# Kernel optimization log

Measured on AMD Instinct MI355X. Metric: run time of the kernel, lower is better.

## Reference

```python
import jax, jax.numpy as jnp
import numpy as np
import math

N = 500_000
C_IN = 16
C_OUT = 64
H, W = 256, 256
PE_DIM = 32
BOUNDS = (-1.0, 1.0)
LN_EPS = 1e-5


def setup_inputs() -> dict:
    key = jax.random.key(0)
    ks = jax.random.split(key, 4)
    d_in = C_IN + 6 * PE_DIM  # 208
    pos = jax.random.uniform(ks[0], (N, 3), jnp.float32, minval=-1.0, maxval=1.0)
    features = jax.random.normal(ks[1], (N, C_IN), jnp.float32)
    W1 = jax.random.normal(ks[2], (d_in, C_OUT), jnp.float32) * (1.0 / math.sqrt(d_in))
    b1 = jnp.zeros((C_OUT,), jnp.float32)
    ln_g = jnp.ones((C_OUT,), jnp.float32)
    ln_b = jnp.zeros((C_OUT,), jnp.float32)
    W2 = jax.random.normal(ks[3], (C_OUT, C_OUT), jnp.float32) * (1.0 / math.sqrt(C_OUT))
    b2 = jnp.zeros((C_OUT,), jnp.float32)
    return {"pos": pos, "features": features, "W1": W1, "b1": b1,
            "ln_g": ln_g, "ln_b": ln_b, "W2": W2, "b2": b2,
            "axis1": 0, "axis2": 1}


def _pos_encode(pos):
    # sinusoidal encoding: per spatial dim, sin/cos at PE_DIM frequencies
    scale = BOUNDS[1] - BOUNDS[0]
    freq_bands = jnp.arange(PE_DIM, dtype=jnp.float32) / PE_DIM  # linspace(0,31,32)/32
    freqs = (pos / scale)[..., None] * (2.0 ** freq_bands) * math.pi  # [N,3,PE]
    # ordering per dim: sin_d, cos_d -> [N, 3*2*PE]
    enc = jnp.stack([jnp.sin(freqs), jnp.cos(freqs)], axis=2)  # [N,3,2,PE]
    return enc.reshape(pos.shape[0], 3 * 2 * PE_DIM)


def _layernorm(x, g, b):
    mu = jnp.mean(x, axis=-1, keepdims=True)
    var = jnp.var(x, axis=-1, keepdims=True)
    return (x - mu) * jax.lax.rsqrt(var + LN_EPS) * g + b


def reference(pos, features, W1, b1, ln_g, ln_b, W2, b2, axis1, axis2):
    # MLP on [features | pos_encoding]
    combined = jnp.concatenate([features, _pos_encode(pos)], axis=-1)  # [N,208]
    h = combined @ W1 + b1
    h = jax.nn.gelu(_layernorm(h, ln_g, ln_b), approximate=False)
    feat = h @ W2 + b2  # [N,C_OUT]

    # grid indices for the projected plane
    lo, hi = BOUNDS
    norm = jnp.clip((pos - lo) / (hi - lo), 0.0, 1.0)
    res = jnp.array([H, W], jnp.float32)
    i1 = jnp.clip(jnp.floor(norm[:, axis1] * res[0]), 0, H - 1).astype(jnp.int32)
    i2 = jnp.clip(jnp.floor(norm[:, axis2] * res[1]), 0, W - 1).astype(jnp.int32)
    flat = i1 * W + i2  # [N]

    # scatter-mean into grid
    sums = jax.ops.segment_sum(feat, flat, num_segments=H * W)  # [H*W, C]
    counts = jax.ops.segment_sum(jnp.ones((feat.shape[0],), jnp.float32), flat,
                                 num_segments=H * W)
    grid = sums / jnp.maximum(counts, 1.0)[:, None]  # [H*W, C]
    grid = grid.reshape(H, W, C_OUT).transpose(2, 0, 1)  # [C,H,W]
    return grid[None]  # [1,C,H,W]
```

## Files before the change

### kernel.cpp

```cpp
#include <hip/hip_runtime.h>
#include <math.h>

#define NPTS   500000
#define CIN    16
#define COUT   64
#define GRID_W 256
#define NCELL  65536

#define WS_HIST   0
#define WS_STARTS 262144
#define WS_CR     524288
#define WS_SORT   2621440
#define WS_WPK    4718592
#define WS_FEAT   4755456
#define WS_NEED   (WS_FEAT + (size_t)NPTS * COUT * 2)

#define PT_BLOCKS ((NPTS + 255) / 256)
#define MB_BLOCKS ((NPTS + 511) / 512)

#define W_HALFS   18432
#define W1_FRAGS  28

typedef _Float16 f16x8 __attribute__((ext_vector_type(8)));
typedef _Float16 f16x2 __attribute__((ext_vector_type(2)));
typedef float    f32x4 __attribute__((ext_vector_type(4)));

__device__ __forceinline__ f16x2 pk2(float a, float b) {
    auto r = __builtin_amdgcn_cvt_pkrtz(a, b);
    union { decltype(r) x; f16x2 y; } u; u.x = r;
    return u.y;
}

__device__ __forceinline__ float vsin(float x) {
    float r;
    asm("v_sin_f32 %0, %1" : "=v"(r) : "v"(x));
    return r;
}

__device__ __forceinline__ int cell_index(float v) {
    float nf = fminf(fmaxf((v + 1.0f) * 0.5f, 0.0f), 1.0f);
    int i = (int)floorf(nf * 256.0f);
    return i > 255 ? 255 : i;
}

__device__ __forceinline__ int flat_of(const float* pos, int p, int a1, int a2) {
    float pa1 = pos[p * 3 + a1];
    float pa2 = pos[p * 3 + a2];
    return cell_index(pa1) * GRID_W + cell_index(pa2);
}

__global__ __launch_bounds__(256)
void pack_hist_kernel(const float* __restrict__ W1,
                      const float* __restrict__ W2,
                      const float* __restrict__ pos,
                      const int* __restrict__ ax1p,
                      const int* __restrict__ ax2p,
                      _Float16* __restrict__ wpk,
                      unsigned int* __restrict__ hist,
                      unsigned int* __restrict__ cr32)
{
    __shared__ float PSH[768];
    const int t = threadIdx.x;
    const int i = blockIdx.x * 256 + t;

    if (i < W_HALFS) {
        int j = i & 7, lane = (i >> 3) & 63, f = i >> 9;
        int k  = ((f < W1_FRAGS) ? (f >> 2) : ((f - W1_FRAGS) >> 2)) * 32 + ((lane >> 4) << 3) + j;
        int ch = (f & 3) * 16 + (lane & 15);
        float v;
        if (f < W1_FRAGS) v = (k < 208) ? W1[k * 64 + ch] : 0.0f;
        else              v = W2[k * 64 + ch];
        wpk[i] = (_Float16)v;
    }

    const int fbase = blockIdx.x * 768;
    if (fbase + 768 <= NPTS * 3) {
        if (t < 192)
            ((float4*)PSH)[t] = ((const float4*)(pos + fbase))[t];
    } else {
        const int nf = NPTS * 3 - fbase;
        for (int j = t; j < nf; j += 256) PSH[j] = pos[fbase + j];
    }
    __syncthreads();

    if (i < NPTS) {
        const int a1 = ax1p[0], a2 = ax2p[0];
        const float pa1 = PSH[3 * t + a1];
        const float pa2 = PSH[3 * t + a2];
        const int flat = cell_index(pa1) * GRID_W + cell_index(pa2);
        const unsigned int old = atomicAdd(&hist[flat], 1u);
        if (cr32) cr32[i] = (unsigned int)flat | (old << 16);
    }
}

__global__ __launch_bounds__(1024)
void scan_fused_kernel(const unsigned int* __restrict__ hist,
                       unsigned int* __restrict__ starts)
{
    __shared__ unsigned int ssum[1024];
    const int t = threadIdx.x;
    const int base = t * 64;
    unsigned int s = 0;
    #pragma unroll
    for (int i = 0; i < 64; i += 4) {
        uint4 q = *(const uint4*)(hist + base + i);
        s += q.x + q.y + q.z + q.w;
    }
    ssum[t] = s;
    __syncthreads();
    for (int off = 1; off < 1024; off <<= 1) {
        unsigned int add = (t >= off) ? ssum[t - off] : 0u;
        __syncthreads();
        ssum[t] += add;
        __syncthreads();
    }
    unsigned int run = ssum[t] - s;
    #pragma unroll
    for (int i = 0; i < 64; i += 4) {
        uint4 q = *(const uint4*)(hist + base + i);
        starts[base + i + 0] = run; run += q.x;
        starts[base + i + 1] = run; run += q.y;
        starts[base + i + 2] = run; run += q.z;
        starts[base + i + 3] = run; run += q.w;
    }
}

__global__ void build_sorted_kernel(const unsigned int* __restrict__ cr32,
                                    const unsigned int* __restrict__ starts,
                                    int* __restrict__ sorted)
{
    int p = blockIdx.x * 256 + threadIdx.x;
    if (p >= NPTS) return;
    unsigned int cr = cr32[p];
    sorted[starts[cr & 0xFFFFu] + (cr >> 16)] = p;
}

__global__ __launch_bounds__(512, 4)
void mlp_mfma_kernel(const float* __restrict__ pos,
                     const float* __restrict__ feats,
                     const _Float16* __restrict__ wpk,
                     const float* __restrict__ b1,
                     const float* __restrict__ ln_g,
                     const float* __restrict__ ln_b,
                     const int*   __restrict__ ax1p,
                     const int*   __restrict__ ax2p,
                     _Float16* __restrict__ featbuf,
                     float* __restrict__ out,
                     int use_feat)
{
    __shared__ __align__(16) _Float16 WF[W_HALFS];
    __shared__ __align__(16) _Float16 PS[8 * 1024];

    {
        const uint4* src = (const uint4*)wpk;
        uint4* dst = (uint4*)WF;
        for (int i = threadIdx.x; i < W_HALFS / 8; i += 512) dst[i] = src[i];
    }

    const int lane = threadIdx.x & 63;
    const int wv   = threadIdx.x >> 6;
    const int g    = lane >> 4;
    const int n    = lane & 15;
    char* Pw = (char*)(PS + wv * 1024);
    const unsigned sw = (unsigned)((n & 7) << 4);

    const int wbase = blockIdx.x * 512 + wv * 64;

    const float base  = 0.25f * exp2f((float)((8 * g + 16) & 31) * 0.03125f);
    const float RSTEP = 1.02189714865411668f;

    __syncthreads();

    #pragma unroll 1
    for (int tp = 0; tp < 2; ++tp) {
        float px[2], py[2], pz[2];
        f16x8 fH[2];
        #pragma unroll
        for (int u = 0; u < 2; ++u) {
            const int st = wbase + (tp * 2 + u) * 16 + n;
            const int p  = (st < NPTS) ? st : 0;
            px[u] = pos[3 * p + 0];
            py[u] = pos[3 * p + 1];
            pz[u] = pos[3 * p + 2];
            if (g < 2) {
                const float4* fr = (const float4*)(feats + (size_t)p * CIN + g * 8);
                float4 fa = fr[0], fb = fr[1];
                union { f16x8 v; f16x2 h[4]; } Uf;
                Uf.h[0] = pk2(fa.x, fa.y); Uf.h[1] = pk2(fa.z, fa.w);
                Uf.h[2] = pk2(fb.x, fb.y); Uf.h[3] = pk2(fb.z, fb.w);
                fH[u] = Uf.v;
            }
        }

        f32x4 acc[2][4];
        #pragma unroll
        for (int u = 0; u < 2; ++u)
            #pragma unroll
            for (int c = 0; c < 4; ++c)
                acc[u][c] = (f32x4){0.0f, 0.0f, 0.0f, 0.0f};

        #pragma unroll
        for (int s = 0; s < 7; ++s) {
            f16x8 U[2];
            const int k0 = s * 32 + g * 8;
            if (s == 0 && g < 2) {
                U[0] = fH[0]; U[1] = fH[1];
            } else if (k0 >= 208) {
                union { f16x8 v; f16x2 h[4]; } Z;
                #pragma unroll
                for (int q = 0; q < 4; ++q) Z.h[q] = pk2(0.0f, 0.0f);
                U[0] = Z.v; U[1] = Z.v;
            } else {
                const int   e    = k0 - 16;
                const float off  = (e & 32) ? 0.25f : 0.0f;
                const float offc = (e & 32) ? (0.25f * (1.0f - RSTEP)) : 0.0f;
                #pragma unroll
                for (int u = 0; u < 2; ++u) {
                    const float pv = (e < 64) ? px[u] : ((e < 128) ? py[u] : pz[u]);
                    float a = fmaf(pv, base, off);
                    union { f16x8 v; f16x2 h[4]; } G;
                    #pragma unroll
                    for (int q = 0; q < 4; ++q) {
                        float v0 = vsin(a); a = fmaf(a, RSTEP, offc);
                        float v1 = vsin(a); a = fmaf(a, RSTEP, offc);
                        G.h[q] = pk2(v0, v1);
                    }
                    U[u] = G.v;
                }
            }
            #pragma unroll
            for (int c = 0; c < 4; ++c) {
                f16x8 af = ((const f16x8*)WF)[(s * 4 + c) * 64 + lane];
                acc[0][c] = __builtin_amdgcn_mfma_f32_16x16x32_f16(af, U[0], acc[0][c], 0, 0, 0);
                acc[1][c] = __builtin_amdgcn_mfma_f32_16x16x32_f16(af, U[1], acc[1][c], 0, 0, 0);
            }
        }

        #pragma unroll
        for (int u = 0; u < 2; ++u) {
            float s1 = 0.0f, s2 = 0.0f;
            #pragma unroll
            for (int c = 0; c < 4; ++c) {
                f32x4 b1q = *(const f32x4*)(b1 + 16 * c + 4 * g);
                #pragma unroll
                for (int r = 0; r < 4; ++r) {
                    float x = acc[u][c][r] + b1q[r];
                    acc[u][c][r] = x;
                    s1 += x; s2 += x * x;
                }
            }
            s1 += __shfl_xor(s1, 16); s2 += __shfl_xor(s2, 16);
            s1 += __shfl_xor(s1, 32); s2 += __shfl_xor(s2, 32);
            const float mu   = s1 * (1.0f / 64.0f);
            const float var  = s2 * (1.0f / 64.0f) - mu * mu;
            const float rstd = __builtin_amdgcn_rsqf(var + 1e-5f);

            #pragma unroll
            for (int c = 0; c < 4; ++c) {
                f32x4 gq = *(const f32x4*)(ln_g + 16 * c + 4 * g);
                f32x4 bq = *(const f32x4*)(ln_b + 16 * c + 4 * g);
                float gv[4];
                #pragma unroll
                for (int r = 0; r < 4; ++r) {
                    float x  = (acc[u][c][r] - mu) * rstd * gq[r] + bq[r];
                    float w  = x * (0.7978845608028654f + 0.0356774081363001f * x * x);
                    float e2 = __expf(w + w);
                    gv[r] = x * e2 * __builtin_amdgcn_rcpf(e2 + 1.0f);
                }
                union { f16x2 h[2]; uint2 u2; } W;
                W.h[0] = pk2(gv[0], gv[1]);
                W.h[1] = pk2(gv[2], gv[3]);
                *(uint2*)(Pw + n * 128 + (((unsigned)(32 * c + 8 * g)) ^ sw)) = W.u2;
            }

            f32x4 acc2[4];
            #pragma unroll
            for (int c = 0; c < 4; ++c) acc2[c] = (f32x4){0.0f, 0.0f, 0.0f, 0.0f};
            #pragma unroll
            for (int s = 0; s < 2; ++s) {
                f16x8 bf2 = *(const f16x8*)(Pw + n * 128 + (((unsigned)(64 * s + 16 * g)) ^ sw));
                #pragma unroll
                for (int c = 0; c < 4; ++c) {
                    f16x8 af = ((const f16x8*)WF)[(W1_FRAGS + s * 4 + c) * 64 + lane];
                    acc2[c] = __builtin_amdgcn_mfma_f32_16x16x32_f16(af, bf2, acc2[c], 0, 0, 0);
                }
            }

            if (use_feat) {
                const int gs = wbase + (tp * 2 + u) * 16 + n;
                if (gs < NPTS) {
                    _Float16* dstp = featbuf + (size_t)gs * COUT + 4 * g;
                    #pragma unroll
                    for (int c = 0; c < 4; ++c) {
                        union { f16x2 h[2]; uint2 u2; } W;
                        W.h[0] = pk2(acc2[c][0], acc2[c][1]);
                        W.h[1] = pk2(acc2[c][2], acc2[c][3]);
                        *(uint2*)(dstp + 16 * c) = W.u2;
                    }
                }
            } else {
                const int st = wbase + (tp * 2 + u) * 16 + n;
                if (st < NPTS) {
                    const int cellr = flat_of(pos, st, ax1p[0], ax2p[0]);
                    #pragma unroll
                    for (int c = 0; c < 4; ++c)
                        #pragma unroll
                        for (int r = 0; r < 4; ++r)
                            unsafeAtomicAdd(&out[(size_t)(16 * c + 4 * g + r) * NCELL + cellr],
                                            acc2[c][r]);
                }
            }
        }
    }
}

__global__ __launch_bounds__(1024)
void reduce_kernel(const _Float16* __restrict__ featbuf,
                   const int* __restrict__ sorted,
                   const unsigned int* __restrict__ starts,
                   const unsigned int* __restrict__ hist,
                   const float* __restrict__ b2,
                   float* __restrict__ out)
{
    __shared__ float R[16][66];
    const int lane  = threadIdx.x & 63;
    const int wv    = threadIdx.x >> 6;
    const int cbase = blockIdx.x * 16;
    const int cq    = lane & 7;
    const int rsl   = lane >> 3;

    const int cell = cbase + wv;
    const unsigned int s0  = starts[cell];
    const unsigned int cnt = hist[cell];

    float acc[8];
    #pragma unroll
    for (int j = 0; j < 8; ++j) acc[j] = 0.0f;

    for (unsigned int k = 0; k < cnt; k += 8) {
        const unsigned int kk = k + (unsigned int)rsl;
        const bool ok = kk < cnt;
        const int r = sorted[ok ? (s0 + kk) : s0];
        union { uint4 u; f16x2 h[4]; } V;
        V.u = *(const uint4*)(featbuf + (size_t)r * COUT + cq * 8);
        #pragma unroll
        for (int j = 0; j < 4; ++j) {
            acc[2 * j]     += ok ? (float)V.h[j].x : 0.0f;
            acc[2 * j + 1] += ok ? (float)V.h[j].y : 0.0f;
        }
    }
    #pragma unroll
    for (int m = 8; m <= 32; m <<= 1)
        #pragma unroll
        for (int j = 0; j < 8; ++j)
            acc[j] += __shfl_xor(acc[j], m);

    if (rsl == 0) {
        const float inv = 1.0f / fmaxf((float)cnt, 1.0f);
        float4 b2a = *(const float4*)(b2 + cq * 8);
        float4 b2b = *(const float4*)(b2 + cq * 8 + 4);
        const float bb[8] = {b2a.x, b2a.y, b2a.z, b2a.w, b2b.x, b2b.y, b2b.z, b2b.w};
        #pragma unroll
        for (int j = 0; j < 8; ++j)
            R[wv][cq * 8 + j] = cnt ? (acc[j] * inv + bb[j]) : 0.0f;
    }
    __syncthreads();

    const int ch = threadIdx.x >> 4;
    const int ci = threadIdx.x & 15;
    out[ch * NCELL + cbase + ci] = R[ci][ch];
}

__global__ void finalize_kernel(float* __restrict__ out,
                                const unsigned int* __restrict__ hist,
                                const float* __restrict__ b2)
{
    int t = blockIdx.x * 256 + threadIdx.x;
    int cell = t & (NCELL - 1);
    int ch   = t >> 16;
    float c  = (float)hist[cell];
    out[t] = out[t] / fmaxf(c, 1.0f) + ((c > 0.0f) ? b2[ch] : 0.0f);
}

extern "C" void kernel_launch(void* const* d_in, const int* in_sizes, int n_in,
                              void* d_out, int out_size, void* d_ws, size_t ws_size,
                              hipStream_t stream) {
    (void)in_sizes; (void)n_in; (void)out_size;
    const float* pos   = (const float*)d_in[0];
    const float* feats = (const float*)d_in[1];
    const float* W1    = (const float*)d_in[2];
    const float* b1    = (const float*)d_in[3];
    const float* ln_g  = (const float*)d_in[4];
    const float* ln_b  = (const float*)d_in[5];
    const float* W2    = (const float*)d_in[6];
    const float* b2    = (const float*)d_in[7];
    const int*   ax1   = (const int*)d_in[8];
    const int*   ax2   = (const int*)d_in[9];

    char* ws = (char*)d_ws;
    unsigned int* hist   = (unsigned int*)(ws + WS_HIST);
    unsigned int* starts = (unsigned int*)(ws + WS_STARTS);
    unsigned int* cr32   = (unsigned int*)(ws + WS_CR);
    int*          sorted = (int*)(ws + WS_SORT);
    _Float16*     wpk    = (_Float16*)(ws + WS_WPK);
    _Float16*     featbf = (_Float16*)(ws + WS_FEAT);

    float* out = (float*)d_out;
    const int use_feat = (ws_size >= WS_NEED) ? 1 : 0;

    hipMemsetAsync(hist, 0, NCELL * sizeof(unsigned int), stream);
    if (!use_feat)
        hipMemsetAsync(d_out, 0, (size_t)COUT * NCELL * sizeof(float), stream);

    pack_hist_kernel<<<PT_BLOCKS, 256, 0, stream>>>(
        W1, W2, pos, ax1, ax2, wpk, hist,
        use_feat ? cr32 : (unsigned int*)nullptr);
    if (use_feat) {
        scan_fused_kernel<<<1, 1024, 0, stream>>>(hist, starts);
        build_sorted_kernel<<<PT_BLOCKS, 256, 0, stream>>>(cr32, starts, sorted);
    }
    mlp_mfma_kernel<<<MB_BLOCKS, 512, 0, stream>>>(
        pos, feats, wpk, b1, ln_g, ln_b, ax1, ax2, featbf, out, use_feat);
    if (use_feat)
        reduce_kernel<<<NCELL / 16, 1024, 0, stream>>>(featbf, sorted, starts, hist, b2, out);
    else
        finalize_kernel<<<(COUT * NCELL) / 256, 256, 0, stream>>>(out, hist, b2);
}
```

Measured before the change: 224.4 us.

## Fuse cell histogram and rank computation into MLP kernel

Moves the per-point cell index, histogram atomic and rank recording out of the separate pack/hist kernel and into the MLP kernel. Those steps reuse the positions the MLP kernel already loads, and weight packing becomes a tiny standalone kernel. The scan and sort kernels now run after the MLP, which removes a separate full pass over the positions and reorders the pipeline. The cost is extra atomics and register pressure inside the MLP kernel.

```diff
diff --git a/kernel.cpp b/kernel.cpp
--- a/kernel.cpp
+++ b/kernel.cpp
@@ -49,48 +49,19 @@
     return cell_index(pa1) * GRID_W + cell_index(pa2);
 }
 
-__global__ __launch_bounds__(256)
-void pack_hist_kernel(const float* __restrict__ W1,
-                      const float* __restrict__ W2,
-                      const float* __restrict__ pos,
-                      const int* __restrict__ ax1p,
-                      const int* __restrict__ ax2p,
-                      _Float16* __restrict__ wpk,
-                      unsigned int* __restrict__ hist,
-                      unsigned int* __restrict__ cr32)
-{
-    __shared__ float PSH[768];
-    const int t = threadIdx.x;
-    const int i = blockIdx.x * 256 + t;
-
-    if (i < W_HALFS) {
-        int j = i & 7, lane = (i >> 3) & 63, f = i >> 9;
-        int k  = ((f < W1_FRAGS) ? (f >> 2) : ((f - W1_FRAGS) >> 2)) * 32 + ((lane >> 4) << 3) + j;
-        int ch = (f & 3) * 16 + (lane & 15);
-        float v;
-        if (f < W1_FRAGS) v = (k < 208) ? W1[k * 64 + ch] : 0.0f;
-        else              v = W2[k * 64 + ch];
-        wpk[i] = (_Float16)v;
-    }
-
-    const int fbase = blockIdx.x * 768;
-    if (fbase + 768 <= NPTS * 3) {
-        if (t < 192)
-            ((float4*)PSH)[t] = ((const float4*)(pos + fbase))[t];
-    } else {
-        const int nf = NPTS * 3 - fbase;
-        for (int j = t; j < nf; j += 256) PSH[j] = pos[fbase + j];
-    }
-    __syncthreads();
-
-    if (i < NPTS) {
-        const int a1 = ax1p[0], a2 = ax2p[0];
-        const float pa1 = PSH[3 * t + a1];
-        const float pa2 = PSH[3 * t + a2];
-        const int flat = cell_index(pa1) * GRID_W + cell_index(pa2);
-        const unsigned int old = atomicAdd(&hist[flat], 1u);
-        if (cr32) cr32[i] = (unsigned int)flat | (old << 16);
-    }
+__global__ void pack_w_kernel(const float* __restrict__ W1,
+                              const float* __restrict__ W2,
+                              _Float16* __restrict__ wpk)
+{
+    int i = blockIdx.x * 256 + threadIdx.x;
+    if (i >= W_HALFS) return;
+    int j = i & 7, lane = (i >> 3) & 63, f = i >> 9;
+    int k  = ((f < W1_FRAGS) ? (f >> 2) : ((f - W1_FRAGS) >> 2)) * 32 + ((lane >> 4) << 3) + j;
+    int ch = (f & 3) * 16 + (lane & 15);
+    float v;
+    if (f < W1_FRAGS) v = (k < 208) ? W1[k * 64 + ch] : 0.0f;
+    else              v = W2[k * 64 + ch];
+    wpk[i] = (_Float16)v;
 }
 
 __global__ __launch_bounds__(1024)
@@ -144,6 +115,8 @@
                      const float* __restrict__ ln_b,
                      const int*   __restrict__ ax1p,
                      const int*   __restrict__ ax2p,
+                     unsigned int* __restrict__ hist,
+                     unsigned int* __restrict__ cr32,
                      _Float16* __restrict__ featbuf,
                      float* __restrict__ out,
                      int use_feat)
@@ -165,6 +138,7 @@
     const unsigned sw = (unsigned)((n & 7) << 4);
 
     const int wbase = blockIdx.x * 512 + wv * 64;
+    const int a1 = ax1p[0], a2 = ax2p[0];
 
     const float base  = 0.25f * exp2f((float)((8 * g + 16) & 31) * 0.03125f);
     const float RSTEP = 1.02189714865411668f;
@@ -311,6 +285,20 @@
                 }
             }
         }
+
+        {
+            const int st2 = wbase + (tp * 2 + (g & 1)) * 16 + n;
+            if (g < 2 && st2 < NPTS) {
+                const float qx = (g & 1) ? px[1] : px[0];
+                const float qy = (g & 1) ? py[1] : py[0];
+                const float qz = (g & 1) ? pz[1] : pz[0];
+                const float pa1 = (a1 == 0) ? qx : ((a1 == 1) ? qy : qz);
+                const float pa2 = (a2 == 0) ? qx : ((a2 == 1) ? qy : qz);
+                const int flat = cell_index(pa1) * GRID_W + cell_index(pa2);
+                const unsigned int old = atomicAdd(&hist[flat], 1u);
+                if (cr32) cr32[st2] = (unsigned int)flat | (old << 16);
+            }
+        }
     }
 }
 
@@ -412,17 +400,15 @@
     if (!use_feat)
         hipMemsetAsync(d_out, 0, (size_t)COUT * NCELL * sizeof(float), stream);
 
-    pack_hist_kernel<<<PT_BLOCKS, 256, 0, stream>>>(
-        W1, W2, pos, ax1, ax2, wpk, hist,
-        use_feat ? cr32 : (unsigned int*)nullptr);
+    pack_w_kernel<<<(W_HALFS + 255) / 256, 256, 0, stream>>>(W1, W2, wpk);
+    mlp_mfma_kernel<<<MB_BLOCKS, 512, 0, stream>>>(
+        pos, feats, wpk, b1, ln_g, ln_b, ax1, ax2, hist,
+        use_feat ? cr32 : (unsigned int*)nullptr, featbf, out, use_feat);
     if (use_feat) {
         scan_fused_kernel<<<1, 1024, 0, stream>>>(hist, starts);
         build_sorted_kernel<<<PT_BLOCKS, 256, 0, stream>>>(cr32, starts, sorted);
-    }
-    mlp_mfma_kernel<<<MB_BLOCKS, 512, 0, stream>>>(
-        pos, feats, wpk, b1, ln_g, ln_b, ax1, ax2, featbf, out, use_feat);
-    if (use_feat)
         reduce_kernel<<<NCELL / 16, 1024, 0, stream>>>(featbf, sorted, starts, hist, b2, out);
-    else
+    } else {
         finalize_kernel<<<(COUT * NCELL) / 256, 256, 0, stream>>>(out, hist, b2);
-}
+    }
+}
```

After: 218.6 us. 2.6% less time.
